# Optimization experiments

Measured on AMD Instinct MI355X. Metric: run time of the kernel, lower is better.

## Reference

```python
import jax, jax.numpy as jnp
import numpy as np

EPS = 1e-5

def layer_norm(x, g, b):
    mu = jnp.mean(x, axis=-1, keepdims=True)
    var = jnp.mean(jnp.square(x - mu), axis=-1, keepdims=True)
    return (x - mu) * jax.lax.rsqrt(var + EPS) * g + b

def setup_inputs() -> dict:
    key = jax.random.key(0)
    ks = jax.random.split(key, 10)
    B, V, S, D, H, FF = 4, 1024, 2048, 512, 8, 2048
    s = 0.02
    return {
        "tgt": jax.random.normal(ks[0], (B, V, D), jnp.float32),
        "memory": jax.random.normal(ks[1], (B, S, D), jnp.float32),
        "memory_key_padding_mask": jax.random.bernoulli(ks[2], 0.3, (B, S)),  # True = padding
        "Wq": jax.random.normal(ks[3], (D, D), jnp.float32) * s,
        "Wkv": jax.random.normal(ks[4], (2 * D, D), jnp.float32) * s,
        "Wo": jax.random.normal(ks[5], (D, D), jnp.float32) * s,
        "W1": jax.random.normal(ks[6], (FF, D), jnp.float32) * s,
        "b1": jnp.zeros((FF,), jnp.float32),
        "W2": jax.random.normal(ks[7], (D, FF), jnp.float32) * s,
        "b2": jnp.zeros((D,), jnp.float32),
        "g1": jnp.ones((D,), jnp.float32),
        "be1": jnp.zeros((D,), jnp.float32),
        "g2": jnp.ones((D,), jnp.float32),
        "be2": jnp.zeros((D,), jnp.float32),
    }

def reference(tgt, memory, memory_key_padding_mask, Wq, Wkv, Wo, W1, b1, W2, b2, g1, be1, g2, be2):
    B, V, D = tgt.shape
    S = memory.shape[1]
    H = 8
    hd = D // H
    # projections (no bias on q/kv/out per bias=False)
    q = (tgt @ Wq.T).reshape(B, V, H, hd)
    kv = (memory @ Wkv.T).reshape(B, S, 2, H, hd)
    k, v = kv[:, :, 0], kv[:, :, 1]
    # cross attention over valid (non-padded) context tokens only.
    # Equivalent math to flash-attn-varlen packing: padded keys get zero weight.
    scores = jnp.einsum("bqhd,bkhd->bhqk", q, k) / jnp.sqrt(jnp.asarray(hd, q.dtype))
    neg = jnp.finfo(scores.dtype).min
    scores = jnp.where(memory_key_padding_mask[:, None, None, :], neg, scores)
    attn = jax.nn.softmax(scores, axis=-1)
    attn_out = jnp.einsum("bhqk,bkhd->bqhd", attn, v).reshape(B, V, D)
    attn_out = attn_out @ Wo.T
    # post-norm scheme, dropout=0
    x = layer_norm(tgt + attn_out, g1, be1)
    ff = jax.nn.relu(x @ W1.T + b1) @ W2.T + b2
    return layer_norm(x + ff, g2, be2)
```

## Files before the change

### kernel.cpp

```cpp
#include <hip/hip_runtime.h>

typedef unsigned short u16;
typedef __attribute__((ext_vector_type(8))) short short8;
typedef __attribute__((ext_vector_type(4))) float floatx4;

#define AS1 __attribute__((address_space(1)))
#define AS3 __attribute__((address_space(3)))

__device__ __forceinline__ u16 f2bf(float f) {
  unsigned u = __float_as_uint(f);
  u = u + 0x7FFFu + ((u >> 16) & 1u);
  return (u16)(u >> 16);
}
__device__ __forceinline__ unsigned pack_bf2(float a, float b) {
  return (unsigned)f2bf(a) | ((unsigned)f2bf(b) << 16);
}

__global__ __launch_bounds__(256) void cast_all_kernel(
    const float* __restrict__ s0, u16* __restrict__ d0,
    const float* __restrict__ s1, u16* __restrict__ d1,
    const float* __restrict__ s2, u16* __restrict__ d2,
    const float* __restrict__ s3, u16* __restrict__ d3,
    const float* __restrict__ s4, u16* __restrict__ d4,
    const float* __restrict__ s5, u16* __restrict__ d5,
    const float* __restrict__ s6, u16* __restrict__ d6)
{
  const int total = 2359296;
  int i = blockIdx.x * 256 + threadIdx.x;
  const int stride = gridDim.x * 256;
  for (; i < total; i += stride) {
    const float* s; u16* d; int loc;
    if (i < 524288)        { s = s0; d = d0; loc = i; }
    else if (i < 1572864)  { s = s1; d = d1; loc = i - 524288; }
    else if (i < 1638400)  { s = s2; d = d2; loc = i - 1572864; }
    else if (i < 1769472)  { s = s3; d = d3; loc = i - 1638400; }
    else if (i < 1835008)  { s = s4; d = d4; loc = i - 1769472; }
    else if (i < 2097152)  { s = s5; d = d5; loc = i - 1835008; }
    else                   { s = s6; d = d6; loc = i - 2097152; }
    float4 v = reinterpret_cast<const float4*>(s)[loc];
    ushort4 o;
    o.x = f2bf(v.x); o.y = f2bf(v.y); o.z = f2bf(v.z); o.w = f2bf(v.w);
    reinterpret_cast<ushort4*>(d)[loc] = o;
  }
}

__global__ __launch_bounds__(256) void mask_bits_kernel(const void* __restrict__ mraw,
                                                        unsigned* __restrict__ mout, int n) {
  __shared__ int mode;
  const int t = threadIdx.x;
  const int* mi = (const int*)mraw;
  if (t == 0) mode = 0;
  __syncthreads();
  int local = 0;
  for (int i = t; i < 2048; i += 256) {
    unsigned v = (unsigned)mi[i];
    if (v == 0x3F800000u) { local = 2; break; }
    if (v > 1u) local = 1;
  }
  atomicMax(&mode, local);
  __syncthreads();
  const int m = mode;
  const uint4* m4 = (const uint4*)mraw;
  const int nw = n / 32;
  for (int wk = t; wk < nw; wk += 256) {
    unsigned bits = 0;
    if (m == 1) {
      uint4 a = m4[wk * 2], b = m4[wk * 2 + 1];
      unsigned ww[8] = {a.x, a.y, a.z, a.w, b.x, b.y, b.z, b.w};
#pragma unroll
      for (int k = 0; k < 8; ++k)
#pragma unroll
        for (int j = 0; j < 4; ++j)
          bits |= (((ww[k] >> (j * 8)) & 0xFFu) ? 1u : 0u) << (k * 4 + j);
    } else {
#pragma unroll
      for (int k = 0; k < 8; ++k) {
        uint4 a = m4[wk * 8 + k];
        unsigned t0 = (m == 2) ? ((a.x << 1) ? 1u : 0u) : (a.x ? 1u : 0u);
        unsigned t1 = (m == 2) ? ((a.y << 1) ? 1u : 0u) : (a.y ? 1u : 0u);
        unsigned t2 = (m == 2) ? ((a.z << 1) ? 1u : 0u) : (a.z ? 1u : 0u);
        unsigned t3 = (m == 2) ? ((a.w << 1) ? 1u : 0u) : (a.w ? 1u : 0u);
        bits |= (t0 | (t1 << 1) | (t2 << 2) | (t3 << 3)) << (k * 4);
      }
    }
    mout[wk] = bits;
  }
}

template<int EPI>
__global__ __launch_bounds__(256) void gemm_bt(
    const u16* __restrict__ A, const u16* __restrict__ B, void* __restrict__ Cv,
    const float* __restrict__ bias,
    int M, int N, int K, int lda, int ldb, int ldc,
    long aBatch, long bBatch, long cBatch)
{
  __shared__ u16 As[2][128 * 32];
  __shared__ u16 Bs[2][128 * 32];
  const int t = threadIdx.x;
  const int l = t & 63;
  const int w = t >> 6;
  const int wr = w >> 1, wc = w & 1;
  const int m0 = blockIdx.y * 128, n0 = blockIdx.x * 128;
  const long z = blockIdx.z;
  const u16* Ab = A + z * aBatch;
  const u16* Bb = B + z * bBatch;

  floatx4 acc[4][4];
#pragma unroll
  for (int m = 0; m < 4; ++m)
#pragma unroll
    for (int n = 0; n < 4; ++n)
      acc[m][n] = (floatx4){0.f, 0.f, 0.f, 0.f};

  const int row_st = t >> 2;
  const int kcol = (t & 3) * 8;

  auto stage = [&](int buf, int kt) {
#pragma unroll
    for (int c = 0; c < 2; ++c) {
      const int rA = m0 + c * 64 + row_st;
      const int rB = n0 + c * 64 + row_st;
      const int li = (c * 256 + t) * 8;
      __builtin_amdgcn_global_load_lds(
          (const AS1 void*)(Ab + (long)rA * lda + kt + kcol),
          (AS3 void*)(As[buf] + li), 16, 0, 0);
      __builtin_amdgcn_global_load_lds(
          (const AS1 void*)(Bb + (long)rB * ldb + kt + kcol),
          (AS3 void*)(Bs[buf] + li), 16, 0, 0);
    }
  };

  stage(0, 0);
  __syncthreads();
  int cur = 0;
  for (int kt = 0; kt < K; kt += 32) {
    if (kt + 32 < K) stage(cur ^ 1, kt + 32);

    short8 af[4], bf[4];
#pragma unroll
    for (int m = 0; m < 4; ++m)
      af[m] = *reinterpret_cast<const short8*>(&As[cur][(wr * 64 + m * 16 + (l & 15)) * 32 + (l >> 4) * 8]);
#pragma unroll
    for (int n = 0; n < 4; ++n)
      bf[n] = *reinterpret_cast<const short8*>(&Bs[cur][(wc * 64 + n * 16 + (l & 15)) * 32 + (l >> 4) * 8]);

    __builtin_amdgcn_s_setprio(1);
#pragma unroll
    for (int m = 0; m < 4; ++m)
#pragma unroll
      for (int n = 0; n < 4; ++n)
        acc[m][n] = __builtin_amdgcn_mfma_f32_16x16x32_bf16(af[m], bf[n], acc[m][n], 0, 0, 0);
    __builtin_amdgcn_s_setprio(0);

    __syncthreads();
    cur ^= 1;
  }

  const int cr = (l >> 4) * 4;
  const int cc = l & 15;
#pragma unroll
  for (int m = 0; m < 4; ++m) {
#pragma unroll
    for (int j = 0; j < 4; ++j) {
      const int row = m0 + wr * 64 + m * 16 + cr + j;
#pragma unroll
      for (int n = 0; n < 4; ++n) {
        const int col = n0 + wc * 64 + n * 16 + cc;
        float v = acc[m][n][j];
        long idx = z * cBatch + (long)row * ldc + col;
        if constexpr (EPI == 0) {
          ((u16*)Cv)[idx] = f2bf(v);
        } else if constexpr (EPI == 1) {
          ((float*)Cv)[idx] = v;
        } else if constexpr (EPI == 2) {
          v += bias[col]; v = fmaxf(v, 0.f);
          ((u16*)Cv)[idx] = f2bf(v);
        } else if constexpr (EPI == 3) {
          v += bias[col];
          ((float*)Cv)[idx] = v;
        } else {
          ((u16*)Cv)[idx] = f2bf(v * 0.125f);
        }
      }
    }
  }
}

__global__ __launch_bounds__(512, 4) void flash_attn_kernel(
    const u16* __restrict__ Qg, const u16* __restrict__ KVg,
    const u16* __restrict__ Vtg, const unsigned* __restrict__ mbits,
    u16* __restrict__ Og)
{
  __shared__ __align__(16) u16 KVbuf[2][2][64 * 64];
  __shared__ __align__(16) u16 Ps[8][16 * 32];
  __shared__ float mlred[2][2][64];
  __shared__ unsigned mw[64];

  const int t = threadIdx.x;
  const int l = t & 63;
  const int w = t >> 6;
  const int wr = w >> 1;
  const int wc = w & 1;
  const int lo = l & 15, hi = l >> 4;

  const int id = blockIdx.y * 16 + blockIdx.x;
  const int vid = (id & 7) * 64 + (id >> 3);
  const int qt = vid & 15, bh = vid >> 4;
  const int b = bh >> 3, h = bh & 7;

  const long qbase = ((long)b * 1024 + qt * 64) * 512 + h * 64;
  const long kbase = ((long)b * 2048) * 1024 + h * 64;
  const long vbase = ((long)bh * 64) * 2048;

  if (t < 64) mw[t] = mbits[b * 64 + t];

  auto stage_kv = [&](int buf, int soff) {
    const int s = t >> 3, c = t & 7;
    __builtin_amdgcn_global_load_lds(
        (const AS1 void*)(KVg + kbase + (long)(soff + s) * 1024 + ((c ^ (s & 7)) * 8)),
        (AS3 void*)(&KVbuf[buf][0][t * 8]), 16, 0, 0);
    __builtin_amdgcn_global_load_lds(
        (const AS1 void*)(Vtg + vbase + (long)s * 2048 + soff + ((c ^ (s & 7)) * 8)),
        (AS3 void*)(&KVbuf[buf][1][t * 8]), 16, 0, 0);
  };

  stage_kv(0, 0);

  short8 af[2];
#pragma unroll
  for (int ks = 0; ks < 2; ++ks)
    af[ks] = *reinterpret_cast<const short8*>(
        Qg + qbase + (long)(wr * 16 + lo) * 512 + ks * 32 + hi * 8);

  __syncthreads();

  floatx4 accO[4];
#pragma unroll
  for (int dn = 0; dn < 4; ++dn)
    accO[dn] = (floatx4){0.f, 0.f, 0.f, 0.f};
  float m_run = -1.0e30f, l_run = 0.f;

  int cur = 0;
  for (int it = 0; it < 32; ++it) {
    const int s0 = it * 64;
    if (it + 1 < 32) stage_kv(cur ^ 1, s0 + 64);

    short8 bfr[2][2];
#pragma unroll
    for (int sn = 0; sn < 2; ++sn)
#pragma unroll
      for (int ks = 0; ks < 2; ++ks) {
        const int srow = wc * 32 + sn * 16 + lo;
        bfr[sn][ks] = *reinterpret_cast<const short8*>(
            &KVbuf[cur][0][srow * 64 + (((ks * 4 + hi) ^ (lo & 7)) * 8)]);
      }
    floatx4 sacc[2];
#pragma unroll
    for (int sn = 0; sn < 2; ++sn)
      sacc[sn] = (floatx4){0.f, 0.f, 0.f, 0.f};
    __builtin_amdgcn_s_setprio(1);
#pragma unroll
    for (int sn = 0; sn < 2; ++sn)
#pragma unroll
      for (int ks = 0; ks < 2; ++ks)
        sacc[sn] = __builtin_amdgcn_mfma_f32_16x16x32_bf16(bfr[sn][ks], af[ks], sacc[sn], 0, 0, 0);
    __builtin_amdgcn_s_setprio(0);

    const unsigned mword = mw[it * 2 + wc];
#pragma unroll
    for (int sn = 0; sn < 2; ++sn) {
      const unsigned nib = (mword >> (sn * 16)) >> (hi * 4);
#pragma unroll
      for (int j = 0; j < 4; ++j)
        if ((nib >> j) & 1u) sacc[sn][j] = -3.0e38f;
    }

    float mx = fmaxf(fmaxf(fmaxf(sacc[0][0], sacc[0][1]), fmaxf(sacc[0][2], sacc[0][3])),
                     fmaxf(fmaxf(sacc[1][0], sacc[1][1]), fmaxf(sacc[1][2], sacc[1][3])));
    mx = fmaxf(mx, __shfl_xor(mx, 16));
    mx = fmaxf(mx, __shfl_xor(mx, 32));
    const float mn = fmaxf(m_run, mx);
    const float al = __expf(m_run - mn);
    m_run = mn;
    l_run *= al;
#pragma unroll
    for (int dn = 0; dn < 4; ++dn)
#pragma unroll
      for (int j = 0; j < 4; ++j)
        accO[dn][j] *= al;

    {
      float s = 0.f;
      unsigned pw[2][2];
#pragma unroll
      for (int sn = 0; sn < 2; ++sn) {
        const float e0 = __expf(sacc[sn][0] - m_run);
        const float e1 = __expf(sacc[sn][1] - m_run);
        const float e2 = __expf(sacc[sn][2] - m_run);
        const float e3 = __expf(sacc[sn][3] - m_run);
        s += (e0 + e1) + (e2 + e3);
        pw[sn][0] = pack_bf2(e0, e1);
        pw[sn][1] = pack_bf2(e2, e3);
      }
      s += __shfl_xor(s, 16);
      s += __shfl_xor(s, 32);
      l_run += s;
#pragma unroll
      for (int sn = 0; sn < 2; ++sn) {
        uint2 wv; wv.x = pw[sn][0]; wv.y = pw[sn][1];
        *reinterpret_cast<uint2*>(&Ps[w][lo * 32 + (((sn * 4 + hi) ^ (lo & 7)) * 4)]) = wv;
      }
    }

    short8 va[4];
#pragma unroll
    for (int dn = 0; dn < 4; ++dn) {
      const int d = dn * 16 + lo;
      va[dn] = *reinterpret_cast<const short8*>(
          &KVbuf[cur][1][d * 64 + (((wc * 4 + hi) ^ (d & 7)) * 8)]);
    }
    short8 pb;
    {
      uint2 a = *reinterpret_cast<const uint2*>(&Ps[w][lo * 32 + (((2 * hi) ^ (lo & 7)) * 4)]);
      uint2 bq = *reinterpret_cast<const uint2*>(&Ps[w][lo * 32 + (((2 * hi + 1) ^ (lo & 7)) * 4)]);
      uint4 comb; comb.x = a.x; comb.y = a.y; comb.z = bq.x; comb.w = bq.y;
      __builtin_memcpy(&pb, &comb, 16);
    }
    __builtin_amdgcn_s_setprio(1);
#pragma unroll
    for (int dn = 0; dn < 4; ++dn)
      accO[dn] = __builtin_amdgcn_mfma_f32_16x16x32_bf16(va[dn], pb, accO[dn], 0, 0, 0);
    __builtin_amdgcn_s_setprio(0);

    __syncthreads();
    cur ^= 1;
  }

  if (hi == 0) {
    const int q = wr * 16 + lo;
    mlred[wc][0][q] = m_run;
    mlred[wc][1][q] = l_run;
  }
  __syncthreads();
  float scal;
  {
    const int q = wr * 16 + lo;
    const float ms = fmaxf(mlred[0][0][q], mlred[1][0][q]);
    scal = __expf(m_run - ms);
  }
  float* Of = (float*)KVbuf;
  if (wc == 0) {
#pragma unroll
    for (int dn = 0; dn < 4; ++dn) {
      const int q = wr * 16 + lo;
      float4 v;
      v.x = accO[dn][0] * scal; v.y = accO[dn][1] * scal;
      v.z = accO[dn][2] * scal; v.w = accO[dn][3] * scal;
      *reinterpret_cast<float4*>(&Of[q * 64 + (((dn * 4 + hi) ^ (q & 15)) * 4)]) = v;
    }
  }
  __syncthreads();
  if (wc == 1) {
#pragma unroll
    for (int dn = 0; dn < 4; ++dn) {
      const int q = wr * 16 + lo;
      float4* pp = reinterpret_cast<float4*>(&Of[q * 64 + (((dn * 4 + hi) ^ (q & 15)) * 4)]);
      float4 v = *pp;
      v.x += accO[dn][0] * scal; v.y += accO[dn][1] * scal;
      v.z += accO[dn][2] * scal; v.w += accO[dn][3] * scal;
      *pp = v;
    }
  }
  __syncthreads();
  {
    const int q = t >> 3;
    const int dc = t & 7;
    const float m0 = mlred[0][0][q], m1 = mlred[1][0][q];
    const float ms = fmaxf(m0, m1);
    const float ls = mlred[0][1][q] * __expf(m0 - ms) + mlred[1][1][q] * __expf(m1 - ms);
    const float inv = 1.0f / ls;
    float4 v0 = *reinterpret_cast<const float4*>(&Of[q * 64 + (((dc * 2) ^ (q & 15)) * 4)]);
    float4 v1 = *reinterpret_cast<const float4*>(&Of[q * 64 + (((dc * 2 + 1) ^ (q & 15)) * 4)]);
    u16 ov[8];
    ov[0] = f2bf(v0.x * inv); ov[1] = f2bf(v0.y * inv);
    ov[2] = f2bf(v0.z * inv); ov[3] = f2bf(v0.w * inv);
    ov[4] = f2bf(v1.x * inv); ov[5] = f2bf(v1.y * inv);
    ov[6] = f2bf(v1.z * inv); ov[7] = f2bf(v1.w * inv);
    uint4 wv;
    __builtin_memcpy(&wv, ov, 16);
    *reinterpret_cast<uint4*>(Og + qbase + (long)q * 512 + dc * 8) = wv;
  }
}

template<int P, bool WRITE_BF>
__global__ __launch_bounds__(64) void lnp_kernel(const float* __restrict__ r1,
    const float* __restrict__ parts, long pstride,
    const float* __restrict__ bias,
    const float* __restrict__ g, const float* __restrict__ be,
    float* __restrict__ xf, u16* __restrict__ xb) {
  const long base = (long)blockIdx.x * 512;
  const int t = threadIdx.x;
  float v[8]; float s = 0.f;
#pragma unroll
  for (int j = 0; j < 8; ++j) {
    int i = t + j * 64;
    float acc = r1[base + i] + (bias ? bias[i] : 0.f);
#pragma unroll
    for (int q = 0; q < P; ++q) acc += parts[q * pstride + base + i];
    v[j] = acc; s += acc;
  }
#pragma unroll
  for (int o = 32; o; o >>= 1) s += __shfl_xor(s, o);
  const float mu = s * (1.0f / 512.0f);
  float q2 = 0.f;
#pragma unroll
  for (int j = 0; j < 8; ++j) { float d = v[j] - mu; q2 += d * d; }
#pragma unroll
  for (int o = 32; o; o >>= 1) q2 += __shfl_xor(q2, o);
  const float rs = rsqrtf(q2 * (1.0f / 512.0f) + 1e-5f);
#pragma unroll
  for (int j = 0; j < 8; ++j) {
    int i = t + j * 64;
    float o = (v[j] - mu) * rs * g[i] + be[i];
    xf[base + i] = o;
    if (WRITE_BF) xb[base + i] = f2bf(o);
  }
}

__global__ __launch_bounds__(256) void transpose_v_kernel(const u16* __restrict__ KV,
                                                          u16* __restrict__ Vt) {
  __shared__ u16 tile[128 * 65];
  const int z = blockIdx.y;
  const int b = z >> 3, h = z & 7;
  const int s0 = blockIdx.x * 128;
  const int t = threadIdx.x;
#pragma unroll
  for (int k = 0; k < 32; ++k) {
    int i = k * 256 + t;
    int s = i >> 6, d = i & 63;
    tile[s * 65 + d] = KV[(long)(b * 2048 + s0 + s) * 1024 + 512 + h * 64 + d];
  }
  __syncthreads();
#pragma unroll
  for (int k = 0; k < 32; ++k) {
    int i = k * 256 + t;
    int d = i >> 7, sl = i & 127;
    Vt[((long)z * 64 + d) * 2048 + s0 + sl] = tile[sl * 65 + d];
  }
}

extern "C" void kernel_launch(void* const* d_in, const int* in_sizes, int n_in,
                              void* d_out, int out_size, void* d_ws, size_t ws_size,
                              hipStream_t stream) {
  const float* tgt    = (const float*)d_in[0];
  const float* memory = (const float*)d_in[1];
  const void*  maskraw= (const void*)d_in[2];
  const float* Wq  = (const float*)d_in[3];
  const float* Wkv = (const float*)d_in[4];
  const float* Wo  = (const float*)d_in[5];
  const float* W1  = (const float*)d_in[6];
  const float* b1  = (const float*)d_in[7];
  const float* W2  = (const float*)d_in[8];
  const float* b2  = (const float*)d_in[9];
  const float* g1  = (const float*)d_in[10];
  const float* be1 = (const float*)d_in[11];
  const float* g2  = (const float*)d_in[12];
  const float* be2 = (const float*)d_in[13];

  constexpr int B = 4, V = 1024, S = 2048, D = 512, H = 8, FF = 2048, hd = 64;
  const long BVD = (long)B * V * D;

  char* p = (char*)d_ws;
  auto alloc = [&](size_t bytes) -> void* {
    void* r = (void*)p; p += (bytes + 255) & ~(size_t)255; return r;
  };
  u16*  tgt_b = (u16*)alloc((size_t)B * V * D * 2);
  u16*  mem_b = (u16*)alloc((size_t)B * S * D * 2);
  u16*  wq_b  = (u16*)alloc((size_t)D * D * 2);
  u16*  wkv_b = (u16*)alloc((size_t)2 * D * D * 2);
  u16*  wo_b  = (u16*)alloc((size_t)D * D * 2);
  u16*  w1_b  = (u16*)alloc((size_t)FF * D * 2);
  u16*  w2_b  = (u16*)alloc((size_t)D * FF * 2);
  u16*  Qb    = (u16*)alloc((size_t)B * V * D * 2);
  u16*  KVb   = (u16*)alloc((size_t)B * S * 2 * D * 2);
  u16*  Vt    = (u16*)alloc((size_t)B * H * hd * S * 2);
  u16*  attn_b= (u16*)alloc((size_t)B * V * D * 2);
  float* projP = (float*)alloc((size_t)4 * BVD * 4);
  float* xf   = (float*)alloc((size_t)BVD * 4);
  u16*  xb    = (u16*)alloc((size_t)BVD * 2);
  u16*  hb    = (u16*)alloc((size_t)B * V * FF * 2);
  float* ffbP = (float*)alloc((size_t)4 * BVD * 4);
  unsigned* mbitsW = (unsigned*)alloc((size_t)(B * S / 32) * 4);

  cast_all_kernel<<<dim3(2048), 256, 0, stream>>>(
      tgt, tgt_b, memory, mem_b, Wq, wq_b, Wkv, wkv_b, Wo, wo_b, W1, w1_b, W2, w2_b);

  mask_bits_kernel<<<dim3(1), 256, 0, stream>>>(maskraw, mbitsW, B * S);

  gemm_bt<4><<<dim3(D / 128, (B * V) / 128, 1), 256, 0, stream>>>(
      tgt_b, wq_b, Qb, nullptr, B * V, D, D, D, D, D, 0, 0, 0);
  gemm_bt<0><<<dim3((2 * D) / 128, (B * S) / 128, 1), 256, 0, stream>>>(
      mem_b, wkv_b, KVb, nullptr, B * S, 2 * D, D, D, D, 2 * D, 0, 0, 0);
  transpose_v_kernel<<<dim3(S / 128, B * H), 256, 0, stream>>>(KVb, Vt);

  flash_attn_kernel<<<dim3(16, B * H), 512, 0, stream>>>(
      Qb, KVb, Vt, mbitsW, attn_b);

  gemm_bt<1><<<dim3(D / 128, (B * V) / 128, 4), 256, 0, stream>>>(
      attn_b, wo_b, projP, nullptr, B * V, D, D / 4, D, D, D,
      (long)(D / 4), (long)(D / 4), BVD);
  lnp_kernel<4, true><<<dim3(B * V), 64, 0, stream>>>(
      tgt, projP, BVD, nullptr, g1, be1, xf, xb);
  gemm_bt<2><<<dim3(FF / 128, (B * V) / 128, 1), 256, 0, stream>>>(
      xb, w1_b, hb, b1, B * V, FF, D, D, D, FF, 0, 0, 0);
  gemm_bt<1><<<dim3(D / 128, (B * V) / 128, 4), 256, 0, stream>>>(
      hb, w2_b, ffbP, nullptr, B * V, D, FF / 4, FF, FF, D,
      (long)(FF / 4), (long)(FF / 4), BVD);
  lnp_kernel<4, false><<<dim3(B * V), 64, 0, stream>>>(
      xf, ffbP, BVD, b2, g2, be2, (float*)d_out, nullptr);
}
```

Measured before the change: 268.5 us.

## Replace split-K GEMMs with 64x64 tile GEMMs and fuse residual epilogues

Adds a 64x64-tile GEMM kernel for the N=512 projections (Q, out-proj, FFN2). It replaces the 4-way split-K fp32 partial buffers with a single pass that adds the residual and bias directly in the epilogue. The layernorm kernels now read one pre-summed buffer, which cuts partial-sum traffic. Flash attention also skips the running-max rescale unless some lane's new max exceeds the old one by more than 8, trading a little exp-range headroom for fewer multiplies.

```diff
diff --git a/kernel.cpp b/kernel.cpp
--- a/kernel.cpp
+++ b/kernel.cpp
@@ -91,8 +91,7 @@
 __global__ __launch_bounds__(256) void gemm_bt(
     const u16* __restrict__ A, const u16* __restrict__ B, void* __restrict__ Cv,
     const float* __restrict__ bias,
-    int M, int N, int K, int lda, int ldb, int ldc,
-    long aBatch, long bBatch, long cBatch)
+    int M, int N, int K, int lda, int ldb, int ldc)
 {
   __shared__ u16 As[2][128 * 32];
   __shared__ u16 Bs[2][128 * 32];
@@ -101,9 +100,6 @@
   const int w = t >> 6;
   const int wr = w >> 1, wc = w & 1;
   const int m0 = blockIdx.y * 128, n0 = blockIdx.x * 128;
-  const long z = blockIdx.z;
-  const u16* Ab = A + z * aBatch;
-  const u16* Bb = B + z * bBatch;
 
   floatx4 acc[4][4];
 #pragma unroll
@@ -122,10 +118,10 @@
       const int rB = n0 + c * 64 + row_st;
       const int li = (c * 256 + t) * 8;
       __builtin_amdgcn_global_load_lds(
-          (const AS1 void*)(Ab + (long)rA * lda + kt + kcol),
+          (const AS1 void*)(A + (long)rA * lda + kt + kcol),
           (AS3 void*)(As[buf] + li), 16, 0, 0);
       __builtin_amdgcn_global_load_lds(
-          (const AS1 void*)(Bb + (long)rB * ldb + kt + kcol),
+          (const AS1 void*)(B + (long)rB * ldb + kt + kcol),
           (AS3 void*)(Bs[buf] + li), 16, 0, 0);
     }
   };
@@ -167,19 +163,95 @@
       for (int n = 0; n < 4; ++n) {
         const int col = n0 + wc * 64 + n * 16 + cc;
         float v = acc[m][n][j];
-        long idx = z * cBatch + (long)row * ldc + col;
+        long idx = (long)row * ldc + col;
         if constexpr (EPI == 0) {
           ((u16*)Cv)[idx] = f2bf(v);
-        } else if constexpr (EPI == 1) {
-          ((float*)Cv)[idx] = v;
-        } else if constexpr (EPI == 2) {
+        } else {
           v += bias[col]; v = fmaxf(v, 0.f);
           ((u16*)Cv)[idx] = f2bf(v);
-        } else if constexpr (EPI == 3) {
-          v += bias[col];
-          ((float*)Cv)[idx] = v;
+        }
+      }
+    }
+  }
+}
+
+template<int EPI>
+__global__ __launch_bounds__(256) void gemm64(
+    const u16* __restrict__ A, const u16* __restrict__ B, void* __restrict__ Cv,
+    const float* __restrict__ res, const float* __restrict__ bias,
+    int K, int lda, int ldb, int ldc)
+{
+  __shared__ u16 As[2][64 * 32];
+  __shared__ u16 Bs[2][64 * 32];
+  const int t = threadIdx.x;
+  const int l = t & 63;
+  const int w = t >> 6;
+  const int wr = w >> 1, wc = w & 1;
+  const int lo = l & 15, hi = l >> 4;
+  const int m0 = blockIdx.y * 64, n0 = blockIdx.x * 64;
+
+  floatx4 acc[2][2];
+#pragma unroll
+  for (int m = 0; m < 2; ++m)
+#pragma unroll
+    for (int n = 0; n < 2; ++n)
+      acc[m][n] = (floatx4){0.f, 0.f, 0.f, 0.f};
+
+  const int row_st = t >> 2;
+  const int kcol = (t & 3) * 8;
+
+  auto stage = [&](int buf, int kt) {
+    __builtin_amdgcn_global_load_lds(
+        (const AS1 void*)(A + (long)(m0 + row_st) * lda + kt + kcol),
+        (AS3 void*)(As[buf] + t * 8), 16, 0, 0);
+    __builtin_amdgcn_global_load_lds(
+        (const AS1 void*)(B + (long)(n0 + row_st) * ldb + kt + kcol),
+        (AS3 void*)(Bs[buf] + t * 8), 16, 0, 0);
+  };
+
+  stage(0, 0);
+  __syncthreads();
+  int cur = 0;
+  for (int kt = 0; kt < K; kt += 32) {
+    if (kt + 32 < K) stage(cur ^ 1, kt + 32);
+
+    short8 af[2], bf[2];
+#pragma unroll
+    for (int m = 0; m < 2; ++m)
+      af[m] = *reinterpret_cast<const short8*>(&As[cur][(wr * 32 + m * 16 + lo) * 32 + hi * 8]);
+#pragma unroll
+    for (int n = 0; n < 2; ++n)
+      bf[n] = *reinterpret_cast<const short8*>(&Bs[cur][(wc * 32 + n * 16 + lo) * 32 + hi * 8]);
+
+    __builtin_amdgcn_s_setprio(1);
+#pragma unroll
+    for (int m = 0; m < 2; ++m)
+#pragma unroll
+      for (int n = 0; n < 2; ++n)
+        acc[m][n] = __builtin_amdgcn_mfma_f32_16x16x32_bf16(af[m], bf[n], acc[m][n], 0, 0, 0);
+    __builtin_amdgcn_s_setprio(0);
+
+    __syncthreads();
+    cur ^= 1;
+  }
+
+  const int cr = hi * 4;
+#pragma unroll
+  for (int m = 0; m < 2; ++m) {
+#pragma unroll
+    for (int j = 0; j < 4; ++j) {
+      const int row = m0 + wr * 32 + m * 16 + cr + j;
+#pragma unroll
+      for (int n = 0; n < 2; ++n) {
+        const int col = n0 + wc * 32 + n * 16 + lo;
+        float v = acc[m][n][j];
+        long idx = (long)row * ldc + col;
+        if constexpr (EPI == 0) {
+          ((u16*)Cv)[idx] = f2bf(v * 0.125f);
+        } else if constexpr (EPI == 1) {
+          ((float*)Cv)[idx] = v + res[idx];
         } else {
-          ((u16*)Cv)[idx] = f2bf(v * 0.125f);
+          ((float*)Cv)[idx] = v + res[idx] + bias[col];
         }
       }
     }
@@ -279,15 +351,17 @@
                      fmaxf(fmaxf(sacc[1][0], sacc[1][1]), fmaxf(sacc[1][2], sacc[1][3])));
     mx = fmaxf(mx, __shfl_xor(mx, 16));
     mx = fmaxf(mx, __shfl_xor(mx, 32));
-    const float mn = fmaxf(m_run, mx);
-    const float al = __expf(m_run - mn);
-    m_run = mn;
-    l_run *= al;
-#pragma unroll
-    for (int dn = 0; dn < 4; ++dn)
-#pragma unroll
-      for (int j = 0; j < 4; ++j)
-        accO[dn][j] *= al;
+    if (!__all(mx <= m_run + 8.0f)) {
+      const float mn = fmaxf(m_run, mx);
+      const float al = __expf(m_run - mn);
+      m_run = mn;
+      l_run *= al;
+#pragma unroll
+      for (int dn = 0; dn < 4; ++dn)
+#pragma unroll
+        for (int j = 0; j < 4; ++j)
+          accO[dn][j] *= al;
+    }
 
     {
       float s = 0.f;
@@ -392,23 +466,15 @@
   }
 }
 
-template<int P, bool WRITE_BF>
-__global__ __launch_bounds__(64) void lnp_kernel(const float* __restrict__ r1,
-    const float* __restrict__ parts, long pstride,
-    const float* __restrict__ bias,
+template<bool WRITE_BF>
+__global__ __launch_bounds__(64) void ln2_kernel(const float* __restrict__ y,
     const float* __restrict__ g, const float* __restrict__ be,
     float* __restrict__ xf, u16* __restrict__ xb) {
   const long base = (long)blockIdx.x * 512;
   const int t = threadIdx.x;
   float v[8]; float s = 0.f;
 #pragma unroll
-  for (int j = 0; j < 8; ++j) {
-    int i = t + j * 64;
-    float acc = r1[base + i] + (bias ? bias[i] : 0.f);
-#pragma unroll
-    for (int q = 0; q < P; ++q) acc += parts[q * pstride + base + i];
-    v[j] = acc; s += acc;
-  }
+  for (int j = 0; j < 8; ++j) { int i = t + j * 64; v[j] = y[base + i]; s += v[j]; }
 #pragma unroll
   for (int o = 32; o; o >>= 1) s += __shfl_xor(s, o);
   const float mu = s * (1.0f / 512.0f);
@@ -474,22 +540,22 @@
   auto alloc = [&](size_t bytes) -> void* {
     void* r = (void*)p; p += (bytes + 255) & ~(size_t)255; return r;
   };
-  u16*  tgt_b = (u16*)alloc((size_t)B * V * D * 2);
+  u16*  tgt_b = (u16*)alloc((size_t)BVD * 2);
   u16*  mem_b = (u16*)alloc((size_t)B * S * D * 2);
   u16*  wq_b  = (u16*)alloc((size_t)D * D * 2);
   u16*  wkv_b = (u16*)alloc((size_t)2 * D * D * 2);
   u16*  wo_b  = (u16*)alloc((size_t)D * D * 2);
   u16*  w1_b  = (u16*)alloc((size_t)FF * D * 2);
   u16*  w2_b  = (u16*)alloc((size_t)D * FF * 2);
-  u16*  Qb    = (u16*)alloc((size_t)B * V * D * 2);
+  u16*  Qb    = (u16*)alloc((size_t)BVD * 2);
   u16*  KVb   = (u16*)alloc((size_t)B * S * 2 * D * 2);
   u16*  Vt    = (u16*)alloc((size_t)B * H * hd * S * 2);
-  u16*  attn_b= (u16*)alloc((size_t)B * V * D * 2);
-  float* projP = (float*)alloc((size_t)4 * BVD * 4);
+  u16*  attn_b= (u16*)alloc((size_t)BVD * 2);
+  float* y1   = (float*)alloc((size_t)BVD * 4);
   float* xf   = (float*)alloc((size_t)BVD * 4);
   u16*  xb    = (u16*)alloc((size_t)BVD * 2);
   u16*  hb    = (u16*)alloc((size_t)B * V * FF * 2);
-  float* ffbP = (float*)alloc((size_t)4 * BVD * 4);
+  float* y2   = (float*)alloc((size_t)BVD * 4);
   unsigned* mbitsW = (unsigned*)alloc((size_t)(B * S / 32) * 4);
 
   cast_all_kernel<<<dim3(2048), 256, 0, stream>>>(
@@ -497,25 +563,21 @@
 
   mask_bits_kernel<<<dim3(1), 256, 0, stream>>>(maskraw, mbitsW, B * S);
 
-  gemm_bt<4><<<dim3(D / 128, (B * V) / 128, 1), 256, 0, stream>>>(
-      tgt_b, wq_b, Qb, nullptr, B * V, D, D, D, D, D, 0, 0, 0);
-  gemm_bt<0><<<dim3((2 * D) / 128, (B * S) / 128, 1), 256, 0, stream>>>(
-      mem_b, wkv_b, KVb, nullptr, B * S, 2 * D, D, D, D, 2 * D, 0, 0, 0);
+  gemm64<0><<<dim3(D / 64, (B * V) / 64), 256, 0, stream>>>(
+      tgt_b, wq_b, Qb, nullptr, nullptr, D, D, D, D);
+  gemm_bt<0><<<dim3((2 * D) / 128, (B * S) / 128), 256, 0, stream>>>(
+      mem_b, wkv_b, KVb, nullptr, B * S, 2 * D, D, D, D, 2 * D);
   transpose_v_kernel<<<dim3(S / 128, B * H), 256, 0, stream>>>(KVb, Vt);
 
   flash_attn_kernel<<<dim3(16, B * H), 512, 0, stream>>>(
       Qb, KVb, Vt, mbitsW, attn_b);
 
-  gemm_bt<1><<<dim3(D / 128, (B * V) / 128, 4), 256, 0, stream>>>(
-      attn_b, wo_b, projP, nullptr, B * V, D, D / 4, D, D, D,
-      (long)(D / 4), (long)(D / 4), BVD);
-  lnp_kernel<4, true><<<dim3(B * V), 64, 0, stream>>>(
-      tgt, projP, BVD, nullptr, g1, be1, xf, xb);
-  gemm_bt<2><<<dim3(FF / 128, (B * V) / 128, 1), 256, 0, stream>>>(
-      xb, w1_b, hb, b1, B * V, FF, D, D, D, FF, 0, 0, 0);
-  gemm_bt<1><<<dim3(D / 128, (B * V) / 128, 4), 256, 0, stream>>>(
-      hb, w2_b, ffbP, nullptr, B * V, D, FF / 4, FF, FF, D,
-      (long)(FF / 4), (long)(FF / 4), BVD);
-  lnp_kernel<4, false><<<dim3(B * V), 64, 0, stream>>>(
-      xf, ffbP, BVD, b2, g2, be2, (float*)d_out, nullptr);
-}
+  gemm64<1><<<dim3(D / 64, (B * V) / 64), 256, 0, stream>>>(
+      attn_b, wo_b, y1, tgt, nullptr, D, D, D, D);
+  ln2_kernel<true><<<dim3(B * V), 64, 0, stream>>>(y1, g1, be1, xf, xb);
+  gemm_bt<2><<<dim3(FF / 128, (B * V) / 128), 256, 0, stream>>>(
+      xb, w1_b, hb, b1, B * V, FF, D, D, D, FF);
+  gemm64<2><<<dim3(D / 64, (B * V) / 64), 256, 0, stream>>>(
+      hb, w2_b, y2, xf, b2, FF, FF, FF, D);
+  ln2_kernel<false><<<dim3(B * V), 64, 0, stream>>>(y2, g2, be2, (float*)d_out, nullptr);
+}
```

Measured after the change: 262.8 us. 1.02x faster.
